# Kernel tuning notes

Hardware: AMD Instinct MI355X
Metric: run time of the kernel (lower is better)

The kernel has to match this reference:

```python
import jax, jax.numpy as jnp
from jax import lax
import numpy as np

STEP = 0.1            # step_size
INC = 1.5             # bracket_expansion_increase
MAX_EXPAND = 16       # fixed cap on bracket-expansion iterations (masked no-ops after convergence)
MAX_SHRINK = 24       # fixed cap on shrinkage-rejection iterations


def setup_inputs() -> dict:
    key = jax.random.key(0)
    kx, kw = jax.random.split(key)
    B, D = 65536, 128
    x = jax.random.normal(kx, (B, D), jnp.float32)
    W = jax.random.normal(kw, (D, D), jnp.float32) / np.float32(np.sqrt(D))
    return {"x": x, "W": W}


def _potential(x, W):
    # correlated Gaussian potential: -0.5 * ||W x||^2, per chain
    z = x @ W.T                      # [B, D]
    return -0.5 * jnp.sum(z * z, axis=-1)  # [B]


def _slice_sample(x, W):
    B = x.shape[0]
    key = jax.random.key(42)
    k_y, k_dir, k_u0, k_shr = jax.random.split(key, 4)

    pot = _potential(x, W)                               # [B]
    # y = log(1 - u) + potential  (log of uniform height under the density)
    y = jnp.log1p(-jax.random.uniform(k_y, pot.shape, jnp.float32)) + pot

    dirs = jax.random.normal(k_dir, x.shape, jnp.float32)
    dirs = dirs / jnp.linalg.norm(dirs, axis=-1, keepdims=True)  # unit slice directions

    mask0 = y < pot

    # --- bracket expansion (lower: sign=-1, upper: sign=+1), masked fixed-trip scan ---
    def expand(sign):
        def body(carry, i):
            b, mask = carry
            step_i = STEP * jnp.power(jnp.float32(INC), i.astype(jnp.float32))
            b = jnp.where(mask, b + sign * step_i, b)
            pot_b = _potential(x + b[:, None] * dirs, W)
            mask = mask & (y < pot_b)
            return (b, mask), None
        (b, _), _ = lax.scan(body, (jnp.zeros((B,), jnp.float32), mask0),
                             jnp.arange(MAX_EXPAND))
        return b

    lb = expand(-1.0)
    ub = expand(+1.0)

    # --- initial proposal on the bracket ---
    u = jax.random.uniform(k_u0, (B,), jnp.float32) * (ub - lb) + lb
    x_new = x + u[:, None] * dirs
    mask = _potential(x_new, W) < y   # rejected chains

    # --- shrinkage loop (masked fixed-trip scan) ---
    def shrink(carry, k):
        u, lb, ub, x_new, mask = carry
        smaller = u < 0
        lb = jnp.where(mask & smaller, u, lb)
        ub = jnp.where(mask & ~smaller, u, ub)
        u_prop = jax.random.uniform(k, (B,), jnp.float32) * (ub - lb) + lb
        u = jnp.where(mask, u_prop, u)
        cand = x + u[:, None] * dirs
        pot_c = _potential(cand, W)
        x_new = jnp.where(mask[:, None], cand, x_new)
        mask = mask & (pot_c < y)
        return (u, lb, ub, x_new, mask), None

    keys = jax.random.split(k_shr, MAX_SHRINK)
    (u, lb, ub, x_new, mask), _ = lax.scan(shrink, (u, lb, ub, x_new, mask), keys)
    return x_new


def reference(x, W):
    return _slice_sample(x, W)
```

## Files before the change

### kernel.cpp

```cpp
#include <hip/hip_runtime.h>
#include <stdint.h>
#include <math.h>


#define BD 128
#define NB 65536
#define WS 132
#define XDS 130

typedef float f32x2 __attribute__((ext_vector_type(2)));

#define PK_FMA_LO(acc, xd, wp) \
  asm("v_pk_fma_f32 %0, %1, %2, %0 op_sel_hi:[1,0,1]" \
      : "+v"(acc) : "v"(xd), "v"(wp))
#define PK_FMA_HI(acc, xd, wp) \
  asm("v_pk_fma_f32 %0, %1, %2, %0 op_sel:[0,1,0] op_sel_hi:[1,1,1]" \
      : "+v"(acc) : "v"(xd), "v"(wp))

__host__ __device__ inline uint32_t rotl32(uint32_t v, int s) {
  return (v << s) | (v >> (32 - s));
}

__host__ __device__ inline void tf2x32(uint32_t k0, uint32_t k1,
                                       uint32_t c0, uint32_t c1,
                                       uint32_t* o0, uint32_t* o1) {
  uint32_t ks2 = k0 ^ k1 ^ 0x1BD11BDAu;
  uint32_t x0 = c0 + k0, x1 = c1 + k1;
#define TFR(r) x0 += x1; x1 = rotl32(x1, (r)); x1 ^= x0;
  TFR(13) TFR(15) TFR(26) TFR(6)
  x0 += k1;  x1 += ks2 + 1u;
  TFR(17) TFR(29) TFR(16) TFR(24)
  x0 += ks2; x1 += k0 + 2u;
  TFR(13) TFR(15) TFR(26) TFR(6)
  x0 += k0;  x1 += k1 + 3u;
  TFR(17) TFR(29) TFR(16) TFR(24)
  x0 += k1;  x1 += ks2 + 4u;
  TFR(13) TFR(15) TFR(26) TFR(6)
  x0 += ks2; x1 += k0 + 5u;
#undef TFR
  *o0 = x0; *o1 = x1;
}

__device__ inline uint32_t jbits(uint32_t k0, uint32_t k1, uint32_t n) {
  uint32_t a, b;
  tf2x32(k0, k1, 0u, n, &a, &b);
  return a ^ b;
}

__device__ inline float u01(uint32_t bits) {
  return __fsub_rn(__uint_as_float((bits >> 9) | 0x3f800000u), 1.0f);
}

__device__ inline float xla_log1p(float x) {
  float u  = __fadd_rn(x, 1.0f);
  float lg = (float)log((double)u);
  float sm = __fmul_rn(__fadd_rn(__fmul_rn(-0.5f, x), 1.0f), x);
  return (fabsf(x) < 1e-4f) ? sm : lg;
}

__device__ inline float xla_erfinv(float x) {
  float xx = __fmul_rn(x, x);
  float w  = -xla_log1p(-xx);
  float p;
  if (w < 5.0f) {
    float ww = __fsub_rn(w, 2.5f);
    p = 2.81022636e-08f;
    p = __fadd_rn(3.43273939e-07f,  __fmul_rn(p, ww));
    p = __fadd_rn(-3.5233877e-06f,  __fmul_rn(p, ww));
    p = __fadd_rn(-4.39150654e-06f, __fmul_rn(p, ww));
    p = __fadd_rn(0.00021858087f,   __fmul_rn(p, ww));
    p = __fadd_rn(-0.00125372503f,  __fmul_rn(p, ww));
    p = __fadd_rn(-0.00417768164f,  __fmul_rn(p, ww));
    p = __fadd_rn(0.246640727f,     __fmul_rn(p, ww));
    p = __fadd_rn(1.50140941f,      __fmul_rn(p, ww));
  } else {
    float ww = __fsub_rn(__fsqrt_rn(w), 3.0f);
    p = -0.000200214257f;
    p = __fadd_rn(0.000100950558f,  __fmul_rn(p, ww));
    p = __fadd_rn(0.00134934322f,   __fmul_rn(p, ww));
    p = __fadd_rn(-0.00367342844f,  __fmul_rn(p, ww));
    p = __fadd_rn(0.00573950773f,   __fmul_rn(p, ww));
    p = __fadd_rn(-0.0076224613f,   __fmul_rn(p, ww));
    p = __fadd_rn(0.00943887047f,   __fmul_rn(p, ww));
    p = __fadd_rn(1.00167406f,      __fmul_rn(p, ww));
    p = __fadd_rn(2.83297682f,      __fmul_rn(p, ww));
  }
  return __fmul_rn(p, x);
}

__device__ __attribute__((always_inline)) inline float potential16(
    const f32x2* __restrict__ xdr, const float* __restrict__ wr, float coef) {
  float z[8] = {0.f, 0.f, 0.f, 0.f, 0.f, 0.f, 0.f, 0.f};
#pragma unroll 2
  for (int q = 0; q < 32; ++q) {
    float4 p01 = *(const float4*)(xdr + q * 4);
    float4 p23 = *(const float4*)(xdr + q * 4 + 2);
    float c0 = __fadd_rn(p01.x, __fmul_rn(coef, p01.y));
    float c1 = __fadd_rn(p01.z, __fmul_rn(coef, p01.w));
    float c2 = __fadd_rn(p23.x, __fmul_rn(coef, p23.y));
    float c3 = __fadd_rn(p23.z, __fmul_rn(coef, p23.w));
#pragma unroll
    for (int m = 0; m < 8; ++m) {
      float4 wv = *(const float4*)(wr + m * (16 * WS) + q * 4);
      z[m] = __fmaf_rn(c0, wv.x, z[m]);
      z[m] = __fmaf_rn(c1, wv.y, z[m]);
      z[m] = __fmaf_rn(c2, wv.z, z[m]);
      z[m] = __fmaf_rn(c3, wv.w, z[m]);
    }
  }
  float pr = 0.0f;
#pragma unroll
  for (int m = 0; m < 8; ++m) pr = __fadd_rn(pr, __fmul_rn(z[m], z[m]));
#pragma unroll
  for (int msk = 32; msk >= 4; msk >>= 1)
    pr = __fadd_rn(pr, __shfl_xor(pr, msk));
  return __fmul_rn(-0.5f, pr);
}

__device__ inline double epsb(float u) {
  double au = fabs((double)u);
  return 4e-4 + 8e-5 * au + 8e-6 * au * au;
}

struct KeyArgs {
  uint32_t ky0, ky1;
  uint32_t ku0, ku1;
  uint32_t kd0, kd1;
  uint32_t ks[48];
};

__global__ __launch_bounds__(1024, 1) void slice_fused_kernel(
    const float* __restrict__ X, const float* __restrict__ Wg,
    float* __restrict__ OUT, KeyArgs ka) {
  __shared__ __align__(16) float Wl[128 * WS];
  __shared__ __align__(16) f32x2 XDl[64 * XDS];

  const int tid   = threadIdx.x;
  const int cbase = blockIdx.x * 64;

  for (int i = tid; i < 128 * 32; i += 1024) {
    int r = i >> 5, q = i & 31;
    *(float4*)&Wl[r * WS + q * 4] = ((const float4*)Wg)[i];
  }
  for (int i = tid; i < 64 * 32; i += 1024) {
    int cc = i >> 5, q = i & 31;
    float4 xv = ((const float4*)(X + (size_t)(cbase + cc) * BD))[q];
    float* b0 = (float*)&XDl[cc * XDS + q * 4];
    b0[0] = xv.x; b0[2] = xv.y; b0[4] = xv.z; b0[6] = xv.w;
  }

  const int wave = tid >> 6, lane = tid & 63;
  const int c    = lane & 3;
  const int j    = lane >> 2;
  const int cl   = wave * 4 + c;
  const uint32_t chain = (uint32_t)(cbase + cl);

  {
    const float LO    = __uint_as_float(0xBF7FFFFFu);
    const float SQRT2 = __uint_as_float(0x3FB504F3u);
    float vm[8];
#pragma unroll
    for (int m = 0; m < 8; ++m) {
      uint32_t n = chain * 128u + (uint32_t)(16 * m + j);
      float f  = u01(jbits(ka.kd0, ka.kd1, n));
      float um = fmaxf(LO, __fadd_rn(__fmul_rn(f, 2.0f), LO));
      vm[m] = __fmul_rn(SQRT2, xla_erfinv(um));
    }
    float pr = 0.0f;
#pragma unroll
    for (int m = 0; m < 8; ++m) pr = __fadd_rn(pr, __fmul_rn(vm[m], vm[m]));
#pragma unroll
    for (int msk = 32; msk >= 4; msk >>= 1)
      pr = __fadd_rn(pr, __shfl_xor(pr, msk));
    float nrm = __fsqrt_rn(pr);
#pragma unroll
    for (int m = 0; m < 8; ++m)
      ((float*)&XDl[cl * XDS + 16 * m + j])[1] = vm[m] / nrm;
  }

  __syncthreads();

  const f32x2* xdr = &XDl[cl * XDS];
  const float* wr  = &Wl[j * WS];

  f32x2 zab[8];
#pragma unroll
  for (int m = 0; m < 8; ++m) zab[m] = (f32x2){0.0f, 0.0f};
#pragma unroll 2
  for (int q = 0; q < 32; ++q) {
    float4 p01 = *(const float4*)(xdr + q * 4);
    float4 p23 = *(const float4*)(xdr + q * 4 + 2);
    f32x2 xd0 = {p01.x, p01.y}, xd1 = {p01.z, p01.w};
    f32x2 xd2 = {p23.x, p23.y}, xd3 = {p23.z, p23.w};
#pragma unroll
    for (int m = 0; m < 8; ++m) {
      const float* wb = wr + m * (16 * WS) + q * 4;
      f32x2 w01 = *(const f32x2*)(wb);
      f32x2 w23 = *(const f32x2*)(wb + 2);
      PK_FMA_LO(zab[m], xd0, w01);
      PK_FMA_HI(zab[m], xd1, w01);
      PK_FMA_LO(zab[m], xd2, w23);
      PK_FMA_HI(zab[m], xd3, w23);
    }
  }

  float pr0 = 0.0f;
#pragma unroll
  for (int m = 0; m < 8; ++m) pr0 = __fadd_rn(pr0, __fmul_rn(zab[m].x, zab[m].x));
#pragma unroll
  for (int msk = 32; msk >= 4; msk >>= 1)
    pr0 = __fadd_rn(pr0, __shfl_xor(pr0, msk));
  float pot0 = __fmul_rn(-0.5f, pr0);

  double gl = 0.0, hl = 0.0;
#pragma unroll
  for (int m = 0; m < 8; ++m) {
    gl += (double)zab[m].x * (double)zab[m].y;
    hl += (double)zab[m].y * (double)zab[m].y;
  }
#pragma unroll
  for (int msk = 32; msk >= 4; msk >>= 1) {
    gl += __shfl_xor(gl, msk);
    hl += __shfl_xor(hl, msk);
  }
  const double g = gl, h = hl;
  const double potd0 = (double)pot0;

  float Uy = u01(jbits(ka.ky0, ka.ky1, chain));
  float y  = __fadd_rn(xla_log1p(-Uy), pot0);
  const double yd = (double)y;
  bool mask0 = (y < pot0);

  float lb = 0.0f, ub = 0.0f;
#pragma unroll 1
  for (int side = 0; side < 2; ++side) {
    bool m = mask0;
    float b = 0.0f, pw = 1.0f;
#pragma unroll 1
    for (int i = 0; i < 16; ++i) {
      if (!__any((int)m)) break;
      float step = __fmul_rn(0.1f, pw);
      pw = __fmul_rn(pw, 1.5f);
      if (m) b = side ? __fadd_rn(b, step) : __fsub_rn(b, step);
      double bd   = (double)b;
      double diff = (potd0 - bd * g - 0.5 * bd * bd * h) - yd;
      bool need = m && (fabs(diff) <= epsb(b));
      float pe = 0.0f;
      if (__any((int)need)) pe = potential16(xdr, wr, b);
      bool cont = need ? (y < pe) : (diff > 0.0);
      m = m && cont;
    }
    if (side == 0) lb = b; else ub = b;
  }

  float U0 = u01(jbits(ka.ku0, ka.ku1, chain));
  float u  = __fadd_rn(__fmul_rn(U0, __fsub_rn(ub, lb)), lb);
  bool rej;
  {
    double ud   = (double)u;
    double diff = (potd0 - ud * g - 0.5 * ud * ud * h) - yd;
    bool need = fabs(diff) <= epsb(u);
    float pe = 0.0f;
    if (__any((int)need)) pe = potential16(xdr, wr, u);
    rej = need ? (pe < y) : (diff < 0.0);
  }

#pragma unroll 1
  for (int t = 0; t < 24; ++t) {
    if (!__any((int)rej)) break;
    if (rej) {
      if (u < 0.0f) lb = u; else ub = u;
      float Ut = u01(jbits(ka.ks[2 * t], ka.ks[2 * t + 1], chain));
      u = __fadd_rn(__fmul_rn(Ut, __fsub_rn(ub, lb)), lb);
    }
    double ud   = (double)u;
    double diff = (potd0 - ud * g - 0.5 * ud * ud * h) - yd;
    bool need = rej && (fabs(diff) <= epsb(u));
    float pe = 0.0f;
    if (__any((int)need)) pe = potential16(xdr, wr, u);
    bool rj = need ? (pe < y) : (diff < 0.0);
    rej = rej && rj;
  }

  float* orow = OUT + (size_t)chain * BD;
#pragma unroll
  for (int hh = 0; hh < 2; ++hh) {
    int q2 = j * 2 + hh;
    float4 p01 = *(const float4*)(xdr + q2 * 4);
    float4 p23 = *(const float4*)(xdr + q2 * 4 + 2);
    float4 o;
    o.x = __fadd_rn(p01.x, __fmul_rn(u, p01.y));
    o.y = __fadd_rn(p01.z, __fmul_rn(u, p01.w));
    o.z = __fadd_rn(p23.x, __fmul_rn(u, p23.y));
    o.w = __fadd_rn(p23.z, __fmul_rn(u, p23.w));
    *(float4*)&orow[q2 * 4] = o;
  }
}

extern "C" void kernel_launch(void* const* d_in, const int* in_sizes, int n_in,
                              void* d_out, int out_size, void* d_ws, size_t ws_size,
                              hipStream_t stream) {
  (void)in_sizes; (void)n_in; (void)d_ws; (void)ws_size; (void)out_size;
  const float* x = (const float*)d_in[0];
  const float* W = (const float*)d_in[1];
  float* out = (float*)d_out;

  const uint32_t R0 = 0u, R1 = 42u;
  uint32_t ky0, ky1, kd0, kd1, ku0, ku1, ksh0, ksh1;
  tf2x32(R0, R1, 0u, 0u, &ky0, &ky1);
  tf2x32(R0, R1, 0u, 1u, &kd0, &kd1);
  tf2x32(R0, R1, 0u, 2u, &ku0, &ku1);
  tf2x32(R0, R1, 0u, 3u, &ksh0, &ksh1);

  KeyArgs ka;
  ka.ky0 = ky0; ka.ky1 = ky1; ka.ku0 = ku0; ka.ku1 = ku1;
  ka.kd0 = kd0; ka.kd1 = kd1;
  for (uint32_t t = 0; t < 24; ++t) {
    uint32_t a, b;
    tf2x32(ksh0, ksh1, 0u, t, &a, &b);
    ka.ks[2 * t] = a; ka.ks[2 * t + 1] = b;
  }

  slice_fused_kernel<<<dim3(NB / 64), dim3(1024), 0, stream>>>(x, W, out, ka);
}
```

Before: 138.6 us.

## Precompute per-chain uniforms across the 16 lanes of each chain, fetch via shuffles

Each chain is handled by 16 lanes, and the random uniforms it needs (the y height, the initial proposal and the 24 shrink draws) used to be generated serially by every lane. Now each lane computes one or two of them up front, deriving the shrink subkeys on device, and the shrink loop fetches its draw with a cross-lane shuffle. This spreads threefry hashing across idle lanes and shrinks the kernel argument struct. The per-lane work is now paid even when the loops exit early, and it adds shuffles. It also reworks the inner matvec loads into paired f32x2 structs, which is mostly cosmetic.

```diff
diff --git a/kernel.cpp b/kernel.cpp
--- a/kernel.cpp
+++ b/kernel.cpp
@@ -9,6 +9,7 @@
 #define XDS 130
 
 typedef float f32x2 __attribute__((ext_vector_type(2)));
+typedef struct { f32x2 lo, hi; } f32x2x2;
 
 #define PK_FMA_LO(acc, xd, wp) \
   asm("v_pk_fma_f32 %0, %1, %2, %0 op_sel_hi:[1,0,1]" \
@@ -126,7 +127,7 @@
   uint32_t ky0, ky1;
   uint32_t ku0, ku1;
   uint32_t kd0, kd1;
-  uint32_t ks[48];
+  uint32_t ksh0, ksh1;
 };
 
 __global__ __launch_bounds__(1024, 1) void slice_fused_kernel(
@@ -155,6 +156,18 @@
   const int cl   = wave * 4 + c;
   const uint32_t chain = (uint32_t)(cbase + cl);
 
+  float uA, uB;
+  {
+    uint32_t a0, a1;
+    tf2x32(ka.ksh0, ka.ksh1, 0u, (uint32_t)j, &a0, &a1);
+    uA = u01(jbits(a0, a1, chain));
+    uint32_t d0, d1;
+    tf2x32(ka.ksh0, ka.ksh1, 0u, 16u + (uint32_t)j, &d0, &d1);
+    uint32_t bk0 = (j < 8) ? d0 : (j == 8 ? ka.ky0 : ka.ku0);
+    uint32_t bk1 = (j < 8) ? d1 : (j == 8 ? ka.ky1 : ka.ku1);
+    uB = u01(jbits(bk0, bk1, chain));
+  }
+
   {
     const float LO    = __uint_as_float(0xBF7FFFFFu);
     const float SQRT2 = __uint_as_float(0x3FB504F3u);
@@ -188,19 +201,15 @@
   for (int m = 0; m < 8; ++m) zab[m] = (f32x2){0.0f, 0.0f};
 #pragma unroll 2
   for (int q = 0; q < 32; ++q) {
-    float4 p01 = *(const float4*)(xdr + q * 4);
-    float4 p23 = *(const float4*)(xdr + q * 4 + 2);
-    f32x2 xd0 = {p01.x, p01.y}, xd1 = {p01.z, p01.w};
-    f32x2 xd2 = {p23.x, p23.y}, xd3 = {p23.z, p23.w};
+    f32x2x2 P0 = *(const f32x2x2*)(xdr + q * 4);
+    f32x2x2 P1 = *(const f32x2x2*)(xdr + q * 4 + 2);
 #pragma unroll
     for (int m = 0; m < 8; ++m) {
-      const float* wb = wr + m * (16 * WS) + q * 4;
-      f32x2 w01 = *(const f32x2*)(wb);
-      f32x2 w23 = *(const f32x2*)(wb + 2);
-      PK_FMA_LO(zab[m], xd0, w01);
-      PK_FMA_HI(zab[m], xd1, w01);
-      PK_FMA_LO(zab[m], xd2, w23);
-      PK_FMA_HI(zab[m], xd3, w23);
+      const f32x2x2 wq = *(const f32x2x2*)(wr + m * (16 * WS) + q * 4);
+      PK_FMA_LO(zab[m], P0.lo, wq.lo);
+      PK_FMA_HI(zab[m], P0.hi, wq.lo);
+      PK_FMA_LO(zab[m], P1.lo, wq.hi);
+      PK_FMA_HI(zab[m], P1.hi, wq.hi);
     }
   }
 
@@ -226,7 +235,7 @@
   const double g = gl, h = hl;
   const double potd0 = (double)pot0;
 
-  float Uy = u01(jbits(ka.ky0, ka.ky1, chain));
+  float Uy = __shfl(uB, c + 32);
   float y  = __fadd_rn(xla_log1p(-Uy), pot0);
   const double yd = (double)y;
   bool mask0 = (y < pot0);
@@ -253,7 +262,7 @@
     if (side == 0) lb = b; else ub = b;
   }
 
-  float U0 = u01(jbits(ka.ku0, ka.ku1, chain));
+  float U0 = __shfl(uB, c + 36);
   float u  = __fadd_rn(__fmul_rn(U0, __fsub_rn(ub, lb)), lb);
   bool rej;
   {
@@ -268,9 +277,9 @@
 #pragma unroll 1
   for (int t = 0; t < 24; ++t) {
     if (!__any((int)rej)) break;
+    float Ut = (t < 16) ? __shfl(uA, c + 4 * t) : __shfl(uB, c + 4 * (t - 16));
     if (rej) {
       if (u < 0.0f) lb = u; else ub = u;
-      float Ut = u01(jbits(ka.ks[2 * t], ka.ks[2 * t + 1], chain));
       u = __fadd_rn(__fmul_rn(Ut, __fsub_rn(ub, lb)), lb);
     }
     double ud   = (double)u;
@@ -306,20 +315,11 @@
   float* out = (float*)d_out;
 
   const uint32_t R0 = 0u, R1 = 42u;
-  uint32_t ky0, ky1, kd0, kd1, ku0, ku1, ksh0, ksh1;
-  tf2x32(R0, R1, 0u, 0u, &ky0, &ky1);
-  tf2x32(R0, R1, 0u, 1u, &kd0, &kd1);
-  tf2x32(R0, R1, 0u, 2u, &ku0, &ku1);
-  tf2x32(R0, R1, 0u, 3u, &ksh0, &ksh1);
-
   KeyArgs ka;
-  ka.ky0 = ky0; ka.ky1 = ky1; ka.ku0 = ku0; ka.ku1 = ku1;
-  ka.kd0 = kd0; ka.kd1 = kd1;
-  for (uint32_t t = 0; t < 24; ++t) {
-    uint32_t a, b;
-    tf2x32(ksh0, ksh1, 0u, t, &a, &b);
-    ka.ks[2 * t] = a; ka.ks[2 * t + 1] = b;
-  }
+  tf2x32(R0, R1, 0u, 0u, &ka.ky0, &ka.ky1);
+  tf2x32(R0, R1, 0u, 1u, &ka.kd0, &ka.kd1);
+  tf2x32(R0, R1, 0u, 2u, &ka.ku0, &ka.ku1);
+  tf2x32(R0, R1, 0u, 3u, &ka.ksh0, &ka.ksh1);
 
   slice_fused_kernel<<<dim3(NB / 64), dim3(1024), 0, stream>>>(x, W, out, ka);
 }
```

After: 140.5 us. Within noise of the previous version (+1.4%).
